# Optimization experiments

Measured on AMD Instinct MI355X. Metric: run time of the kernel, lower is better.

Reference implementation:

```python
import jax, jax.numpy as jnp
import numpy as np

N_EMBD = 768
N_HEAD = 8
HEAD_DIM = N_EMBD // N_HEAD
EPS = 1e-5


def _layernorm(x, g, b):
    mu = jnp.mean(x, axis=-1, keepdims=True)
    var = jnp.mean(jnp.square(x - mu), axis=-1, keepdims=True)
    return (x - mu) * jax.lax.rsqrt(var + EPS) * g + b


def _new_gelu(x):
    c = jnp.sqrt(2.0 / jnp.pi).astype(x.dtype)
    return 0.5 * x * (1.0 + jnp.tanh(c * (x + 0.044715 * x * x * x)))


def setup_inputs() -> dict:
    key = jax.random.key(0)
    ks = jax.random.split(key, 10)
    B, T, C = 16, 1024, N_EMBD
    s = lambda fan_in: 1.0 / np.sqrt(fan_in)
    inp = {
        "x": jax.random.normal(ks[0], (B, T, C), dtype=jnp.float32),
        "ln1_g": jnp.ones((C,), jnp.float32),
        "ln1_b": jnp.zeros((C,), jnp.float32),
        "attn_w": jax.random.normal(ks[1], (C, 3 * C), jnp.float32) * s(C),
        "attn_b": jnp.zeros((3 * C,), jnp.float32),
        "proj_w": jax.random.normal(ks[2], (C, C), jnp.float32) * s(C),
        "proj_b": jnp.zeros((C,), jnp.float32),
        "ln2_g": jnp.ones((C,), jnp.float32),
        "ln2_b": jnp.zeros((C,), jnp.float32),
        "fc_w": jax.random.normal(ks[3], (C, 4 * C), jnp.float32) * s(C),
        "fc_b": jnp.zeros((4 * C,), jnp.float32),
        "fc2_w": jax.random.normal(ks[4], (4 * C, C), jnp.float32) * s(4 * C),
        "fc2_b": jnp.zeros((C,), jnp.float32),
    }
    return inp


def reference(x, ln1_g, ln1_b, attn_w, attn_b, proj_w, proj_b,
              ln2_g, ln2_b, fc_w, fc_b, fc2_w, fc2_b):
    B, T, C = x.shape
    H, D = N_HEAD, HEAD_DIM
    scale = 1.0 / np.sqrt(D)

    # --- attention branch ---
    h = _layernorm(x, ln1_g, ln1_b)
    qkv = h @ attn_w + attn_b                       # [B,T,3C]
    q, k, v = jnp.split(qkv, 3, axis=-1)
    q = q.reshape(B, T, H, D).transpose(0, 2, 1, 3)  # [B,H,T,D]
    k = k.reshape(B, T, H, D).transpose(0, 2, 1, 3)
    v = v.reshape(B, T, H, D).transpose(0, 2, 1, 3)
    att = jnp.einsum("bhqd,bhkd->bhqk", q, k) * scale
    causal = jnp.tril(jnp.ones((T, T), bool))
    att = jnp.where(causal, att, -jnp.inf)
    att = jax.nn.softmax(att, axis=-1)
    y = jnp.einsum("bhqk,bhkd->bhqd", att, v)        # [B,H,T,D]
    y = y.transpose(0, 2, 1, 3).reshape(B, T, C)
    y = y @ proj_w + proj_b
    x = x + y

    # --- MLP branch ---
    h2 = _layernorm(x, ln2_g, ln2_b)
    h2 = _new_gelu(h2 @ fc_w + fc_b)
    x = x + (h2 @ fc2_w + fc2_b)
    return x
```

## Files before the change

### kernel.cpp

```cpp
#include <hip/hip_runtime.h>


typedef __bf16 bf16;
typedef __bf16 bf16x8 __attribute__((ext_vector_type(8)));
typedef __bf16 bf16x4 __attribute__((ext_vector_type(4)));
typedef __bf16 bf16x2 __attribute__((ext_vector_type(2)));
typedef float f32x4 __attribute__((ext_vector_type(4)));

__device__ __forceinline__ void async_copy16(const void* g, void* l)
{
    __builtin_amdgcn_global_load_lds((__attribute__((address_space(1))) void*)g,
                                     (__attribute__((address_space(3))) void*)l,
                                     16, 0, 0);
}

__device__ __forceinline__ void bar_nodrain()
{
    __builtin_amdgcn_sched_barrier(0);
    __asm__ volatile("" ::: "memory");
    __builtin_amdgcn_s_barrier();
    __asm__ volatile("" ::: "memory");
    __builtin_amdgcn_sched_barrier(0);
}

__global__ __launch_bounds__(256) void wtrans4(const float* __restrict__ aw, bf16* __restrict__ awT,
                                               const float* __restrict__ pw, bf16* __restrict__ pwT,
                                               const float* __restrict__ fw, bf16* __restrict__ fwT,
                                               const float* __restrict__ f2w, bf16* __restrict__ f2wT)
{
    __shared__ float tile[32][33];
    int id = blockIdx.x;
    const float* in; bf16* out; int R, C, nx;
    if (id < 1728)      { in = aw;  out = awT;  R = 768;  C = 2304; nx = 72; }
    else if (id < 2304) { in = pw;  out = pwT;  R = 768;  C = 768;  nx = 24; id -= 1728; }
    else if (id < 4608) { in = fw;  out = fwT;  R = 768;  C = 3072; nx = 96; id -= 2304; }
    else                { in = f2w; out = f2wT; R = 3072; C = 768;  nx = 24; id -= 4608; }
    const int c0 = (id % nx) * 32, r0 = (id / nx) * 32;
    const int tx = threadIdx.x, ty = threadIdx.y;
#pragma unroll
    for (int i = 0; i < 4; ++i)
        tile[ty + i * 8][tx] = in[(size_t)(r0 + ty + i * 8) * C + c0 + tx];
    __syncthreads();
#pragma unroll
    for (int i = 0; i < 4; ++i)
        out[(size_t)(c0 + ty + i * 8) * R + r0 + tx] = (bf16)tile[tx][ty + i * 8];
}

template <typename TIN>
__global__ __launch_bounds__(256) void ln_kernel(const TIN* __restrict__ x,
                                                 const float* __restrict__ g,
                                                 const float* __restrict__ bb,
                                                 bf16* __restrict__ out)
{
    const int wave = threadIdx.x >> 6, lane = threadIdx.x & 63;
    const size_t row = (size_t)blockIdx.x * 4 + wave;
    const TIN* xr = x + row * 768;
    float v[12];
    float s = 0.f;
    if constexpr (sizeof(TIN) == 2) {
        const bf16x8 t8 = *(const bf16x8*)(xr + lane * 8);
        const bf16x4 t4 = *(const bf16x4*)(xr + 512 + lane * 4);
#pragma unroll
        for (int j = 0; j < 8; ++j) { v[j] = (float)t8[j]; s += v[j]; }
#pragma unroll
        for (int j = 0; j < 4; ++j) { v[8 + j] = (float)t4[j]; s += v[8 + j]; }
    } else {
#pragma unroll
        for (int c = 0; c < 3; ++c) {
            const float4 t4 = *(const float4*)(xr + c * 256 + lane * 4);
            v[c * 4 + 0] = t4.x; v[c * 4 + 1] = t4.y;
            v[c * 4 + 2] = t4.z; v[c * 4 + 3] = t4.w;
            s += t4.x + t4.y + t4.z + t4.w;
        }
    }
#pragma unroll
    for (int off = 32; off >= 1; off >>= 1) s += __shfl_xor(s, off, 64);
    const float mu = s * (1.f / 768.f);
    float q = 0.f;
#pragma unroll
    for (int i = 0; i < 12; ++i) { const float d = v[i] - mu; q += d * d; }
#pragma unroll
    for (int off = 32; off >= 1; off >>= 1) q += __shfl_xor(q, off, 64);
    const float rs = rsqrtf(q * (1.f / 768.f) + 1e-5f);

    if constexpr (sizeof(TIN) == 2) {
        bf16x8 o8; bf16x4 o4;
#pragma unroll
        for (int j = 0; j < 8; ++j) {
            const float gv = g[lane * 8 + j], bv = bb[lane * 8 + j];
            o8[j] = (bf16)((v[j] - mu) * rs * gv + bv);
        }
#pragma unroll
        for (int j = 0; j < 4; ++j) {
            const float gv = g[512 + lane * 4 + j], bv = bb[512 + lane * 4 + j];
            o4[j] = (bf16)((v[8 + j] - mu) * rs * gv + bv);
        }
        *(bf16x8*)(out + row * 768 + lane * 8) = o8;
        *(bf16x4*)(out + row * 768 + 512 + lane * 4) = o4;
    } else {
#pragma unroll
        for (int c = 0; c < 3; ++c) {
            const float4 gv = *(const float4*)(g + c * 256 + lane * 4);
            const float4 bv = *(const float4*)(bb + c * 256 + lane * 4);
            bf16x4 ov;
            ov[0] = (bf16)((v[c * 4 + 0] - mu) * rs * gv.x + bv.x);
            ov[1] = (bf16)((v[c * 4 + 1] - mu) * rs * gv.y + bv.y);
            ov[2] = (bf16)((v[c * 4 + 2] - mu) * rs * gv.z + bv.z);
            ov[3] = (bf16)((v[c * 4 + 3] - mu) * rs * gv.w + bv.w);
            *(bf16x4*)(out + row * 768 + c * 256 + lane * 4) = ov;
        }
    }
}

template <int EPI, int TN>
__global__ __launch_bounds__(256) void gemm_bt(const bf16* __restrict__ A,
                                               const bf16* __restrict__ Bt,
                                               const float* __restrict__ bias,
                                               const void* __restrict__ res,
                                               void* __restrict__ out,
                                               const int M, const int N, const int K)
{
    constexpr int NT_W = TN / 32;
    constexpr int NCPB = (TN * 8) / 256;
    __shared__ bf16 sA[2 * 128 * 32];
    __shared__ bf16 sB[2 * TN * 32];
    const int t = threadIdx.x;
    const int wave = t >> 6, lane = t & 63;
    const int quad = lane >> 4, l16 = lane & 15;
    const int bm0 = blockIdx.x * 128, bn0 = blockIdx.y * TN;
    const int wm = (wave >> 1) * 64, wn = (wave & 1) * (TN / 2);

    const f32x4 z4 = {0.f, 0.f, 0.f, 0.f};
    f32x4 acc[4][NT_W];
#pragma unroll
    for (int i = 0; i < 4; ++i)
#pragma unroll
        for (int j = 0; j < NT_W; ++j) acc[i][j] = z4;

    const bf16* gAp[4]; bf16* lAp[4];
#pragma unroll
    for (int c = 0; c < 4; ++c) {
        const int j = c * 256 + t;
        const int img = j >> 9, r = (j >> 2) & 127, k8 = j & 3;
        gAp[c] = A + (size_t)(bm0 + r) * K + img * 32 + k8 * 8;
        lAp[c] = sA + j * 8;
    }
    const bf16* gBp[NCPB]; bf16* lBp[NCPB];
#pragma unroll
    for (int c = 0; c < NCPB; ++c) {
        const int j = c * 256 + t;
        const int img = j / (TN * 4), r = (j % (TN * 4)) >> 2, k8 = j & 3;
        gBp[c] = Bt + (size_t)(bn0 + r) * K + img * 32 + k8 * 8;
        lBp[c] = sB + j * 8;
    }

    for (int kt = 0; kt < K; kt += 64) {
        __syncthreads();
#pragma unroll
        for (int c = 0; c < 4; ++c) async_copy16(gAp[c] + kt, lAp[c]);
#pragma unroll
        for (int c = 0; c < NCPB; ++c) async_copy16(gBp[c] + kt, lBp[c]);
        __syncthreads();

#pragma unroll
        for (int ks = 0; ks < 2; ++ks) {
            bf16x8 af[4], bfm[NT_W];
#pragma unroll
            for (int mt = 0; mt < 4; ++mt)
                af[mt] = *(const bf16x8*)(sA + ks * 4096 +
                                          (wm + mt * 16 + l16) * 32 + quad * 8);
#pragma unroll
            for (int nt = 0; nt < NT_W; ++nt)
                bfm[nt] = *(const bf16x8*)(sB + ks * (TN * 32) +
                                           (wn + nt * 16 + l16) * 32 + quad * 8);
#pragma unroll
            for (int mt = 0; mt < 4; ++mt)
#pragma unroll
                for (int nt = 0; nt < NT_W; ++nt)
                    acc[mt][nt] = __builtin_amdgcn_mfma_f32_16x16x32_bf16(
                        af[mt], bfm[nt], acc[mt][nt], 0, 0, 0);
        }
    }

    const int rb = bm0 + wm + quad * 4;
    const int cb = bn0 + wn + l16;
#pragma unroll
    for (int mt = 0; mt < 4; ++mt) {
#pragma unroll
        for (int nt = 0; nt < NT_W; ++nt) {
            const int col = cb + nt * 16;
            const float bv = bias[col];
#pragma unroll
            for (int reg = 0; reg < 4; ++reg) {
                const size_t idx = (size_t)(rb + mt * 16 + reg) * N + col;
                float v = acc[mt][nt][reg] + bv;
                if constexpr (EPI == 1) {
                    ((bf16*)out)[idx] = (bf16)(v + ((const float*)res)[idx]);
                } else if constexpr (EPI == 2) {
                    const float u = v;
                    const float a2 = 1.5957691216057308f *
                                     (u + 0.044715f * u * u * u);
                    v = u / (1.f + __expf(-a2));
                    ((bf16*)out)[idx] = (bf16)v;
                } else if constexpr (EPI == 3) {
                    ((float*)out)[idx] = v + (float)((const bf16*)res)[idx];
                } else {
                    ((bf16*)out)[idx] = (bf16)v;
                }
            }
        }
    }
}

template <int EPI>
__global__ __launch_bounds__(512) void gemm256(const bf16* __restrict__ A,
                                               const bf16* __restrict__ Bt,
                                               const float* __restrict__ bias,
                                               bf16* __restrict__ out,
                                               const int M, const int N, const int K)
{
    __shared__ bf16 sA[2][256 * 72];
    __shared__ bf16 sB[2][128 * 72];
    const int t = threadIdx.x;
    const int wave = t >> 6, lane = t & 63;
    const int quad = lane >> 4, l16 = lane & 15;
    const int bm0 = blockIdx.x * 256, bn0 = blockIdx.y * 128;
    const int wm = (wave >> 1) * 64, wn = (wave & 1) * 64;

    const f32x4 z4 = {0.f, 0.f, 0.f, 0.f};
    f32x4 acc[4][4];
#pragma unroll
    for (int i = 0; i < 4; ++i)
#pragma unroll
        for (int j = 0; j < 4; ++j) acc[i][j] = z4;

    const bf16* gA[4]; int lA[4];
#pragma unroll
    for (int c = 0; c < 4; ++c) {
        const int j = c * 512 + t, r = j >> 3, ch = j & 7;
        gA[c] = A + (size_t)(bm0 + r) * K + ch * 8;
        lA[c] = r * 72 + ch * 8;
    }
    const bf16* gB[2]; int lB[2];
#pragma unroll
    for (int c = 0; c < 2; ++c) {
        const int j = c * 512 + t, r = j >> 3, ch = j & 7;
        gB[c] = Bt + (size_t)(bn0 + r) * K + ch * 8;
        lB[c] = r * 72 + ch * 8;
    }

    bf16x8 ra[4], rbv[2];
    auto prefetch = [&](const int kt) {
#pragma unroll
        for (int c = 0; c < 4; ++c) ra[c] = *(const bf16x8*)(gA[c] + kt);
#pragma unroll
        for (int c = 0; c < 2; ++c) rbv[c] = *(const bf16x8*)(gB[c] + kt);
    };
    auto commit = [&](const int buf) {
#pragma unroll
        for (int c = 0; c < 4; ++c) *(bf16x8*)(&sA[buf][lA[c]]) = ra[c];
#pragma unroll
        for (int c = 0; c < 2; ++c) *(bf16x8*)(&sB[buf][lB[c]]) = rbv[c];
    };

    prefetch(0);
    commit(0);
    if (64 < K) prefetch(64);
    __asm__ volatile("s_waitcnt lgkmcnt(0)" ::: "memory");
    bar_nodrain();

    int cur = 0;
    for (int kt = 0; kt < K; kt += 64) {
        if (kt + 64 < K) {
            commit(cur ^ 1);
            if (kt + 128 < K) prefetch(kt + 128);
        }

        __builtin_amdgcn_s_setprio(1);
#pragma unroll
        for (int ks = 0; ks < 2; ++ks) {
            bf16x8 af[4], bfr[4];
#pragma unroll
            for (int mt = 0; mt < 4; ++mt)
                af[mt] = *(const bf16x8*)(&sA[cur][(wm + mt * 16 + l16) * 72 +
                                                   ks * 32 + quad * 8]);
#pragma unroll
            for (int nt = 0; nt < 4; ++nt)
                bfr[nt] = *(const bf16x8*)(&sB[cur][(wn + nt * 16 + l16) * 72 +
                                                    ks * 32 + quad * 8]);
#pragma unroll
            for (int mt = 0; mt < 4; ++mt)
#pragma unroll
                for (int nt = 0; nt < 4; ++nt)
                    acc[mt][nt] = __builtin_amdgcn_mfma_f32_16x16x32_bf16(
                        af[mt], bfr[nt], acc[mt][nt], 0, 0, 0);
        }
        __builtin_amdgcn_s_setprio(0);

        __asm__ volatile("s_waitcnt lgkmcnt(0)" ::: "memory");
        bar_nodrain();
        cur ^= 1;
    }

    const int rb0 = bm0 + wm + quad * 4;
    const int cb = bn0 + wn + l16;
#pragma unroll
    for (int mt = 0; mt < 4; ++mt) {
#pragma unroll
        for (int nt = 0; nt < 4; ++nt) {
            const int col = cb + nt * 16;
            const float bv = bias[col];
#pragma unroll
            for (int reg = 0; reg < 4; ++reg) {
                const size_t idx = (size_t)(rb0 + mt * 16 + reg) * N + col;
                float v = acc[mt][nt][reg] + bv;
                if constexpr (EPI == 2) {
                    const float a2 = 1.5957691216057308f *
                                     (v + 0.044715f * v * v * v);
                    v = v / (1.f + __expf(-a2));
                }
                out[idx] = (bf16)v;
            }
        }
    }
}

__global__ __launch_bounds__(256) void attn_kernel(const bf16* __restrict__ qkv,
                                                   bf16* __restrict__ aout)
{
    constexpr int T = 1024, C3 = 2304, HD = 96, CC = 768;
    __shared__ bf16 sK[64 * 104];
    __shared__ bf16 sV[96 * 72];
    __shared__ bf16 sP[4][16 * 76];
    const int tid = threadIdx.x;
    const int wave = tid >> 6, lane = tid & 63;
    const int quad = lane >> 4, l16 = lane & 15;
    const int bh = blockIdx.x, b = bh >> 3, h = bh & 7;
    const float scale = 0.10206207261596575f;

    const int qAi = blockIdx.y;
    const int qBi = 15 - qAi;
    const int q0A = qAi * 64 + wave * 16;
    const int q0B = qBi * 64 + wave * 16;

    const bf16* kgbase = qkv + (size_t)b * T * C3 + CC + h * HD;
    const bf16* vgbase = qkv + (size_t)b * T * C3 + 2 * CC + h * HD;
    bf16* sPw = &sP[wave][0];

    int kKey[3], kCh[3], vKey2[3], vDq[3];
#pragma unroll
    for (int c = 0; c < 3; ++c) {
        const int j = c * 256 + tid;
        kKey[c] = j / 12; kCh[c] = j - kKey[c] * 12;
        vKey2[c] = (j & 31) * 2; vDq[c] = j >> 5;
    }

    const bf16* qrA = qkv + (size_t)(b * T + q0A + l16) * C3 + h * HD + quad * 8;
    const bf16* qrB = qkv + (size_t)(b * T + q0B + l16) * C3 + h * HD + quad * 8;
    const bf16x8 aQA0 = *(const bf16x8*)(qrA);
    const bf16x8 aQA1 = *(const bf16x8*)(qrA + 32);
    const bf16x8 aQA2 = *(const bf16x8*)(qrA + 64);
    const bf16x8 aQB0 = *(const bf16x8*)(qrB);
    const bf16x8 aQB1 = *(const bf16x8*)(qrB + 32);
    const bf16x8 aQB2 = *(const bf16x8*)(qrB + 64);

    const f32x4 z4 = {0.f, 0.f, 0.f, 0.f};
    f32x4 oA[6], oB[6];
#pragma unroll
    for (int i = 0; i < 6; ++i) { oA[i] = z4; oB[i] = z4; }
    float lA[4] = {0.f, 0.f, 0.f, 0.f}, lB[4] = {0.f, 0.f, 0.f, 0.f};

    bf16x8 kreg[3];
    bf16x4 va[3], vb[3];
    auto issue_tile = [&](const int kk0) {
#pragma unroll
        for (int c = 0; c < 3; ++c) {
            kreg[c] = *(const bf16x8*)(kgbase + (size_t)(kk0 + kKey[c]) * C3 +
                                       kCh[c] * 8);
            const bf16* p0 = vgbase + (size_t)(kk0 + vKey2[c]) * C3 + vDq[c] * 4;
            va[c] = *(const bf16x4*)p0;
            vb[c] = *(const bf16x4*)(p0 + C3);
        }
    };

    auto process = [&](const bf16x8& Q0, const bf16x8& Q1, const bf16x8& Q2,
                       f32x4 (&o)[6], float (&lrow)[4],
                       const int q0, const int kk0, const bool diag) {
        f32x4 s[4];
#pragma unroll
        for (int i = 0; i < 4; ++i) s[i] = z4;
#pragma unroll
        for (int nt = 0; nt < 4; ++nt) {
            const bf16* kp = sK + (nt * 16 + l16) * 104 + quad * 8;
            const bf16x8 b0 = *(const bf16x8*)(kp);
            const bf16x8 b1 = *(const bf16x8*)(kp + 32);
            const bf16x8 b2 = *(const bf16x8*)(kp + 64);
            s[nt] = __builtin_amdgcn_mfma_f32_16x16x32_bf16(Q0, b0, s[nt], 0, 0, 0);
            s[nt] = __builtin_amdgcn_mfma_f32_16x16x32_bf16(Q1, b1, s[nt], 0, 0, 0);
            s[nt] = __builtin_amdgcn_mfma_f32_16x16x32_bf16(Q2, b2, s[nt], 0, 0, 0);
        }

        float psum[4] = {0.f, 0.f, 0.f, 0.f};
#pragma unroll
        for (int nt = 0; nt < 4; ++nt)
#pragma unroll
            for (int reg = 0; reg < 4; ++reg) {
                float v = s[nt][reg] * scale;
                if (diag) {
                    const int qr = q0 + quad * 4 + reg;
                    const int key = kk0 + nt * 16 + l16;
                    v = (key > qr) ? -1e30f : v;
                }
                const float p = __expf(fminf(v, 30.f));
                s[nt][reg] = p;
                psum[reg] += p;
            }

#pragma unroll
        for (int nt = 0; nt < 4; ++nt)
#pragma unroll
            for (int reg = 0; reg < 4; ++reg)
                sPw[(quad * 4 + reg) * 76 + nt * 16 + l16] = (bf16)s[nt][reg];
        __asm__ volatile("s_waitcnt lgkmcnt(0)" ::: "memory");

#pragma unroll
        for (int off = 1; off < 16; off <<= 1)
#pragma unroll
            for (int reg = 0; reg < 4; ++reg)
                psum[reg] += __shfl_xor(psum[reg], off, 64);
#pragma unroll
        for (int reg = 0; reg < 4; ++reg) lrow[reg] += psum[reg];

        const bf16x8 aP0 = *(const bf16x8*)(sPw + l16 * 76 + quad * 8);
        const bf16x8 aP1 = *(const bf16x8*)(sPw + l16 * 76 + 32 + quad * 8);
#pragma unroll
        for (int dd = 0; dd < 6; ++dd) {
            const bf16* vp = sV + (dd * 16 + l16) * 72 + quad * 8;
            const bf16x8 v0 = *(const bf16x8*)(vp);
            const bf16x8 v1 = *(const bf16x8*)(vp + 32);
            o[dd] = __builtin_amdgcn_mfma_f32_16x16x32_bf16(aP0, v0, o[dd], 0, 0, 0);
            o[dd] = __builtin_amdgcn_mfma_f32_16x16x32_bf16(aP1, v1, o[dd], 0, 0, 0);
        }
    };

    issue_tile(0);

    for (int kb = 0; kb <= qBi; ++kb) {
        const int kk0 = kb * 64;

        bar_nodrain();

#pragma unroll
        for (int c = 0; c < 3; ++c)
            *(bf16x8*)(sK + kKey[c] * 104 + kCh[c] * 8) = kreg[c];
#pragma unroll
        for (int c = 0; c < 3; ++c) {
#pragma unroll
            for (int jj = 0; jj < 4; ++jj) {
                bf16x2 pk; pk[0] = va[c][jj]; pk[1] = vb[c][jj];
                *(bf16x2*)(sV + (vDq[c] * 4 + jj) * 72 + vKey2[c]) = pk;
            }
        }

        if (kb < qBi) issue_tile(kk0 + 64);

        __asm__ volatile("s_waitcnt lgkmcnt(0)" ::: "memory");
        bar_nodrain();

        process(aQB0, aQB1, aQB2, oB, lB, q0B, kk0, kb == qBi);
        if (kb <= qAi)
            process(aQA0, aQA1, aQA2, oA, lA, q0A, kk0, kb == qAi);
    }

    bf16* opA = aout + (size_t)(b * T + q0A + quad * 4) * CC + h * HD + l16;
    bf16* opB = aout + (size_t)(b * T + q0B + quad * 4) * CC + h * HD + l16;
#pragma unroll
    for (int reg = 0; reg < 4; ++reg) {
        const float invA = 1.f / lA[reg];
        const float invB = 1.f / lB[reg];
#pragma unroll
        for (int dd = 0; dd < 6; ++dd) {
            opA[(size_t)reg * CC + dd * 16] = (bf16)(oA[dd][reg] * invA);
            opB[(size_t)reg * CC + dd * 16] = (bf16)(oB[dd][reg] * invB);
        }
    }
}

extern "C" void kernel_launch(void* const* d_in, const int* in_sizes, int n_in,
                              void* d_out, int out_size, void* d_ws, size_t ws_size,
                              hipStream_t stream)
{
    const float* x      = (const float*)d_in[0];
    const float* ln1_g  = (const float*)d_in[1];
    const float* ln1_b  = (const float*)d_in[2];
    const float* attn_w = (const float*)d_in[3];
    const float* attn_b = (const float*)d_in[4];
    const float* proj_w = (const float*)d_in[5];
    const float* proj_b = (const float*)d_in[6];
    const float* ln2_g  = (const float*)d_in[7];
    const float* ln2_b  = (const float*)d_in[8];
    const float* fc_w   = (const float*)d_in[9];
    const float* fc_b   = (const float*)d_in[10];
    const float* fc2_w  = (const float*)d_in[11];
    const float* fc2_b  = (const float*)d_in[12];

    char* ws = (char*)d_ws;
    bf16*  attn_wT = (bf16*)(ws + 0);
    bf16*  proj_wT = (bf16*)(ws + 3538944);
    bf16*  fc_wT   = (bf16*)(ws + 4718592);
    bf16*  fc2_wT  = (bf16*)(ws + 9437184);
    bf16*  hbuf    = (bf16*)(ws + 14155776);
    bf16*  qkv     = (bf16*)(ws + 39321600);
    bf16*  x1      = (bf16*)(ws + 39321600);
    bf16*  act     = (bf16*)(ws + 64487424);

    wtrans4<<<6912, dim3(32, 8), 0, stream>>>(attn_w, attn_wT, proj_w, proj_wT,
                                              fc_w, fc_wT, fc2_w, fc2_wT);

    ln_kernel<float><<<4096, 256, 0, stream>>>(x, ln1_g, ln1_b, hbuf);

    gemm256<0><<<dim3(64, 18), 512, 0, stream>>>(
        hbuf, attn_wT, attn_b, qkv, 16384, 2304, 768);

    attn_kernel<<<dim3(128, 8), 256, 0, stream>>>(qkv, hbuf);

    gemm_bt<1, 128><<<dim3(128, 6), 256, 0, stream>>>(
        hbuf, proj_wT, proj_b, x, x1, 16384, 768, 768);

    ln_kernel<bf16><<<4096, 256, 0, stream>>>(x1, ln2_g, ln2_b, hbuf);

    for (int c = 0; c < 2; ++c) {
        const size_t ro = (size_t)c * 8192;
        gemm256<2><<<dim3(32, 24), 512, 0, stream>>>(
            hbuf + ro * 768, fc_wT, fc_b, act, 8192, 3072, 768);
        gemm_bt<3, 64><<<dim3(64, 12), 256, 0, stream>>>(
            act, fc2_wT, fc2_b, x1 + ro * 768,
            (float*)d_out + ro * 768, 8192, 768, 3072);
    }
}
```

Before: 598.3 us.

## Enlarge gemm256 tile to 256x256 with 8x4 per-wave MFMA blocking

Changes the gemm256 block tile from 256x128 to 256x256, so each of the 8 waves computes a 128x64 sub-tile with 32 accumulators, and halves the grid along N for the QKV and FC GEMMs. It also switches the LDS row pitch from 72 to 68 elements, which forces the shared-memory stores and reads to be split into 8-byte halves. The goal is more MFMA work per LDS load and less global traffic for B. The cost is more accumulator registers (lower occupancy), twice the LDS footprint, more LDS instructions from the narrower accesses, and fewer blocks in flight (576 blocks for QKV, 384 per FC launch).

```diff
diff --git a/kernel.cpp b/kernel.cpp
--- a/kernel.cpp
+++ b/kernel.cpp
@@ -219,48 +219,53 @@
                                                bf16* __restrict__ out,
                                                const int M, const int N, const int K)
 {
-    __shared__ bf16 sA[2][256 * 72];
-    __shared__ bf16 sB[2][128 * 72];
+    constexpr int LDW = 68;
+    __shared__ bf16 sA[2][256 * LDW];
+    __shared__ bf16 sB[2][256 * LDW];
     const int t = threadIdx.x;
     const int wave = t >> 6, lane = t & 63;
     const int quad = lane >> 4, l16 = lane & 15;
-    const int bm0 = blockIdx.x * 256, bn0 = blockIdx.y * 128;
-    const int wm = (wave >> 1) * 64, wn = (wave & 1) * 64;
+    const int bm0 = blockIdx.x * 256, bn0 = blockIdx.y * 256;
+    const int wm = (wave >> 2) * 128, wn = (wave & 3) * 64;
 
     const f32x4 z4 = {0.f, 0.f, 0.f, 0.f};
-    f32x4 acc[4][4];
-#pragma unroll
-    for (int i = 0; i < 4; ++i)
+    f32x4 acc[8][4];
+#pragma unroll
+    for (int i = 0; i < 8; ++i)
 #pragma unroll
         for (int j = 0; j < 4; ++j) acc[i][j] = z4;
 
     const bf16* gA[4]; int lA[4];
+    const bf16* gB[4]; int lB[4];
 #pragma unroll
     for (int c = 0; c < 4; ++c) {
         const int j = c * 512 + t, r = j >> 3, ch = j & 7;
         gA[c] = A + (size_t)(bm0 + r) * K + ch * 8;
-        lA[c] = r * 72 + ch * 8;
-    }
-    const bf16* gB[2]; int lB[2];
-#pragma unroll
-    for (int c = 0; c < 2; ++c) {
-        const int j = c * 512 + t, r = j >> 3, ch = j & 7;
         gB[c] = Bt + (size_t)(bn0 + r) * K + ch * 8;
-        lB[c] = r * 72 + ch * 8;
-    }
-
-    bf16x8 ra[4], rbv[2];
+        lA[c] = r * LDW + ch * 8;
+        lB[c] = r * LDW + ch * 8;
+    }
+
+    bf16x8 ra[4], rb[4];
     auto prefetch = [&](const int kt) {
 #pragma unroll
-        for (int c = 0; c < 4; ++c) ra[c] = *(const bf16x8*)(gA[c] + kt);
-#pragma unroll
-        for (int c = 0; c < 2; ++c) rbv[c] = *(const bf16x8*)(gB[c] + kt);
+        for (int c = 0; c < 4; ++c) {
+            ra[c] = *(const bf16x8*)(gA[c] + kt);
+            rb[c] = *(const bf16x8*)(gB[c] + kt);
+        }
     };
     auto commit = [&](const int buf) {
 #pragma unroll
-        for (int c = 0; c < 4; ++c) *(bf16x8*)(&sA[buf][lA[c]]) = ra[c];
-#pragma unroll
-        for (int c = 0; c < 2; ++c) *(bf16x8*)(&sB[buf][lB[c]]) = rbv[c];
+        for (int c = 0; c < 4; ++c) {
+            bf16x4 alo = __builtin_shufflevector(ra[c], ra[c], 0, 1, 2, 3);
+            bf16x4 ahi = __builtin_shufflevector(ra[c], ra[c], 4, 5, 6, 7);
+            *(bf16x4*)(&sA[buf][lA[c]]) = alo;
+            *(bf16x4*)(&sA[buf][lA[c] + 4]) = ahi;
+            bf16x4 blo = __builtin_shufflevector(rb[c], rb[c], 0, 1, 2, 3);
+            bf16x4 bhi = __builtin_shufflevector(rb[c], rb[c], 4, 5, 6, 7);
+            *(bf16x4*)(&sB[buf][lB[c]]) = blo;
+            *(bf16x4*)(&sB[buf][lB[c] + 4]) = bhi;
+        }
     };
 
     prefetch(0);
@@ -279,21 +284,28 @@
         __builtin_amdgcn_s_setprio(1);
 #pragma unroll
         for (int ks = 0; ks < 2; ++ks) {
-            bf16x8 af[4], bfr[4];
-#pragma unroll
-            for (int mt = 0; mt < 4; ++mt)
-                af[mt] = *(const bf16x8*)(&sA[cur][(wm + mt * 16 + l16) * 72 +
-                                                   ks * 32 + quad * 8]);
-#pragma unroll
-            for (int nt = 0; nt < 4; ++nt)
-                bfr[nt] = *(const bf16x8*)(&sB[cur][(wn + nt * 16 + l16) * 72 +
-                                                    ks * 32 + quad * 8]);
-#pragma unroll
-            for (int mt = 0; mt < 4; ++mt)
+            bf16x8 bfr[4];
+#pragma unroll
+            for (int nt = 0; nt < 4; ++nt) {
+                const bf16* p = &sB[cur][(wn + nt * 16 + l16) * LDW +
+                                         ks * 32 + quad * 8];
+                const bf16x4 lo = *(const bf16x4*)p;
+                const bf16x4 hi = *(const bf16x4*)(p + 4);
+                bfr[nt] = __builtin_shufflevector(lo, hi, 0, 1, 2, 3, 4, 5, 6, 7);
+            }
+#pragma unroll
+            for (int mt = 0; mt < 8; ++mt) {
+                const bf16* p = &sA[cur][(wm + mt * 16 + l16) * LDW +
+                                         ks * 32 + quad * 8];
+                const bf16x4 lo = *(const bf16x4*)p;
+                const bf16x4 hi = *(const bf16x4*)(p + 4);
+                const bf16x8 af =
+                    __builtin_shufflevector(lo, hi, 0, 1, 2, 3, 4, 5, 6, 7);
 #pragma unroll
                 for (int nt = 0; nt < 4; ++nt)
                     acc[mt][nt] = __builtin_amdgcn_mfma_f32_16x16x32_bf16(
-                        af[mt], bfr[nt], acc[mt][nt], 0, 0, 0);
+                        af, bfr[nt], acc[mt][nt], 0, 0, 0);
+            }
         }
         __builtin_amdgcn_s_setprio(0);
 
@@ -305,7 +317,7 @@
     const int rb0 = bm0 + wm + quad * 4;
     const int cb = bn0 + wn + l16;
 #pragma unroll
-    for (int mt = 0; mt < 4; ++mt) {
+    for (int mt = 0; mt < 8; ++mt) {
 #pragma unroll
         for (int nt = 0; nt < 4; ++nt) {
             const int col = cb + nt * 16;
@@ -519,7 +531,7 @@
 
     ln_kernel<float><<<4096, 256, 0, stream>>>(x, ln1_g, ln1_b, hbuf);
 
-    gemm256<0><<<dim3(64, 18), 512, 0, stream>>>(
+    gemm256<0><<<dim3(64, 9), 512, 0, stream>>>(
         hbuf, attn_wT, attn_b, qkv, 16384, 2304, 768);
 
     attn_kernel<<<dim3(128, 8), 256, 0, stream>>>(qkv, hbuf);
@@ -531,7 +543,7 @@
 
     for (int c = 0; c < 2; ++c) {
         const size_t ro = (size_t)c * 8192;
-        gemm256<2><<<dim3(32, 24), 512, 0, stream>>>(
+        gemm256<2><<<dim3(32, 12), 512, 0, stream>>>(
             hbuf + ro * 768, fc_wT, fc_b, act, 8192, 3072, 768);
         gemm_bt<3, 64><<<dim3(64, 12), 256, 0, stream>>>(
             act, fc2_wT, fc2_b, x1 + ro * 768,
```

Result: no change. 600.6 us (+0.4%).
